# Performance work log

Measured on AMD Instinct MI355X. Metric: run time of the kernel, lower is better.

## Reference

```python
import jax, jax.numpy as jnp
import numpy as np

B, N, E, H = 16, 196, 512, 8   # batch, tokens(14x14), embedding_channels(=KV_size_S), heads
HD = E // H                    # 64  spatial-attn head dim
C = 4 * E                      # 2048 = KV_size (concat of 4 branches)
HDC = C // H                   # 256 channel-attn (SelfAttentionTAT) head dim

def _ln(x, g, b, eps=1e-6):
    m = jnp.mean(x, -1, keepdims=True)
    v = jnp.mean(jnp.square(x - m), -1, keepdims=True)
    return (x - m) * jax.lax.rsqrt(v + eps) * g + b

def setup_inputs():
    key = jax.random.key(0)
    ks = jax.random.split(key, 16)
    n = lambda k, s, sc=0.02: jax.random.normal(k, s, jnp.float32) * sc
    return {
        "emb1": jax.random.normal(ks[0], (B, N, E), jnp.float32),
        "emb2": jax.random.normal(ks[1], (B, N, E), jnp.float32),
        "emb3": jax.random.normal(ks[2], (B, N, E), jnp.float32),
        "emb4": jax.random.normal(ks[3], (B, N, E), jnp.float32),
        "ln_attn_g": jnp.ones((4, E), jnp.float32), "ln_attn_b": jnp.zeros((4, E), jnp.float32),
        "lnC_g": jnp.ones((C,), jnp.float32), "lnC_b": jnp.zeros((C,), jnp.float32),
        "Wq_c": n(ks[4], (C, C)), "Wk_c": n(ks[5], (C, C)),
        "Wv_c": n(ks[6], (C, C)), "Wo_c": n(ks[7], (C, C)),
        "q_w": n(ks[8], (4, N, N), 0.05),              # query1..4 stacked (token-mixing Linear(196,196))
        "k_w": n(ks[9], (4 * N, 4 * N)),               # key   Linear(784,784)
        "v_w": n(ks[10], (4 * N, 4 * N)),              # value Linear(784,784)
        "out_w": n(ks[11], (4, E, E)),                 # out1..4 stacked
        "ln_ffn_g": jnp.ones((4, E), jnp.float32), "ln_ffn_b": jnp.zeros((4, E), jnp.float32),
        "fc1_w": n(ks[12], (4, E, 4 * E)), "fc1_b": n(ks[13], (4, 4 * E), 1e-6),
        "fc2_w": n(ks[14], (4, 4 * E, E)), "fc2_b": n(ks[15], (4, E), 1e-6),
    }

def reference(emb1, emb2, emb3, emb4, ln_attn_g, ln_attn_b, lnC_g, lnC_b,
              Wq_c, Wk_c, Wv_c, Wo_c, q_w, k_w, v_w, out_w,
              ln_ffn_g, ln_ffn_b, fc1_w, fc1_b, fc2_w, fc2_b):
    embs = jnp.stack([emb1, emb2, emb3, emb4])                         # [4,B,N,E]
    cx = _ln(embs, ln_attn_g[:, None, None, :], ln_attn_b[:, None, None, :])
    ec = _ln(jnp.concatenate([emb1, emb2, emb3, emb4], -1), lnC_g, lnC_b)  # [B,N,C]
    # SelfAttentionTAT: multi-head self-attention over the concatenated channel embedding
    q = (ec @ Wq_c).reshape(B, N, H, HDC).transpose(0, 2, 1, 3)
    k = (ec @ Wk_c).reshape(B, N, H, HDC).transpose(0, 2, 1, 3)
    v = (ec @ Wv_c).reshape(B, N, H, HDC).transpose(0, 2, 1, 3)
    s = jax.nn.softmax(jnp.einsum('bhnd,bhmd->bhnm', q, k) * np.float32(1.0 / np.sqrt(HDC)), -1)
    T_hat = jnp.einsum('bhnm,bhmd->bhnd', s, v).transpose(0, 2, 1, 3).reshape(B, N, C) @ Wo_c
    # split channel dim into 4 chunks, concat along token axis -> [B,4N,E]
    KV_S = T_hat.reshape(B, N, 4, E).transpose(0, 2, 1, 3).reshape(B, 4 * N, E)
    # token-mixing projections (Linear applied to the token axis)
    Q = jnp.einsum('gbnc,gnm->gbmc', cx, q_w)                          # [4,B,N,E]
    K = jnp.einsum('bnc,nm->bmc', KV_S, k_w)                           # [B,4N,E]
    V = jnp.einsum('bnc,nm->bmc', KV_S, v_w)
    Qh = Q.reshape(4, B, N, H, HD).transpose(0, 1, 3, 2, 4)            # [4,B,H,N,HD]
    Kh = K.reshape(B, 4 * N, H, HD).transpose(0, 2, 1, 3)              # [B,H,4N,HD]
    Vh = V.reshape(B, 4 * N, H, HD).transpose(0, 2, 1, 3)
    attn = jnp.einsum('gbhnd,bhmd->gbhnm', Qh, Kh)                     # [4,B,H,N,4N]
    # InstanceNorm2d (no affine, eps=1e-5) over (N,4N) per (branch,batch,head) instead of 1/sqrt(d)
    m = jnp.mean(attn, (-2, -1), keepdims=True)
    var = jnp.mean(jnp.square(attn - m), (-2, -1), keepdims=True)
    p = jax.nn.softmax((attn - m) * jax.lax.rsqrt(var + 1e-5), -1)
    ctx = jnp.einsum('gbhnm,bhmd->gbhnd', p, Vh)                       # [4,B,H,N,HD]
    # faithful to source: only branch 1 is permuted before .view; branches 2-4
    # are .view'ed directly from [B,H,N,HD] (head-major flatten)
    c1 = ctx[0].transpose(0, 2, 1, 3).reshape(B, N, E)
    crest = ctx[1:].reshape(3, B, N, E)
    cmerged = jnp.concatenate([c1[None], crest], 0)                    # [4,B,N,E]
    h = embs + jnp.einsum('gbne,gef->gbnf', cmerged, out_w)            # residual 1
    x = _ln(h, ln_ffn_g[:, None, None, :], ln_ffn_b[:, None, None, :])
    x = jax.nn.gelu(jnp.einsum('gbne,gef->gbnf', x, fc1_w) + fc1_b[:, None, None, :], approximate=False)
    x = jnp.einsum('gbnf,gfe->gbne', x, fc2_w) + fc2_b[:, None, None, :]
    out = x + h                                                        # residual 2
    return (out[0], out[1], out[2], out[3])
```

## Files before the change

### kernel.cpp

```cpp
#include <hip/hip_runtime.h>
#include <hip/hip_bf16.h>
#include <math.h>

typedef __hip_bfloat16 bf16;
typedef __attribute__((ext_vector_type(8))) short v8s;
typedef __attribute__((ext_vector_type(4))) short v4s;
typedef __attribute__((ext_vector_type(4))) float v4f;

#define Bq   16
#define Nq   196
#define Eq   512
#define Hq   8
#define HDq  64
#define Cq   2048
#define HDCq 256
#define N4q  784
#define BNq  (Bq*Nq)
#define SLOT ((long)BNq*Cq)
#define L2E  1.44269504f

struct P4 { const void* p[4]; };

__global__ __launch_bounds__(256) void k_fill(float* __restrict__ out, long n, float v) {
  long i = (long)blockIdx.x * 256 + threadIdx.x;
  if (i < n) out[i] = v;
}

__device__ __forceinline__ float blk_sum(float v, float* buf) {
  #pragma unroll
  for (int off = 32; off; off >>= 1) v += __shfl_down(v, off, 64);
  int tid = threadIdx.x;
  __syncthreads();
  if ((tid & 63) == 0) buf[tid >> 6] = v;
  __syncthreads();
  return buf[0] + buf[1] + buf[2] + buf[3];
}

__device__ __forceinline__ unsigned int pack2bf(float a, float b) {
  unsigned short ha = __builtin_bit_cast(unsigned short, (bf16)a);
  unsigned short hb = __builtin_bit_cast(unsigned short, (bf16)b);
  return (unsigned int)ha | ((unsigned int)hb << 16);
}

__global__ __launch_bounds__(256) void k_ln_concat(
    const float* __restrict__ e1, const float* __restrict__ e2,
    const float* __restrict__ e3, const float* __restrict__ e4,
    const float* __restrict__ gamma, const float* __restrict__ beta,
    bf16* __restrict__ ec) {
  __shared__ float buf[4];
  int row = blockIdx.x;
  int tid = threadIdx.x;
  float vals[8];
  #pragma unroll
  for (int i = 0; i < 8; i++) {
    const float* src = (i < 2) ? e1 : (i < 4) ? e2 : (i < 6) ? e3 : e4;
    vals[i] = src[(long)row * Eq + (i & 1) * 256 + tid];
  }
  float s = 0;
  #pragma unroll
  for (int i = 0; i < 8; i++) s += vals[i];
  float mean = blk_sum(s, buf) * (1.f / 2048.f);
  float ss = 0;
  #pragma unroll
  for (int i = 0; i < 8; i++) { float d = vals[i] - mean; ss += d * d; }
  float rstd = rsqrtf(blk_sum(ss, buf) * (1.f / 2048.f) + 1e-6f);
  #pragma unroll
  for (int i = 0; i < 8; i++) {
    int c = tid + i * 256;
    ec[(long)row * Cq + c] = (bf16)((vals[i] - mean) * rstd * gamma[c] + beta[c]);
  }
}

__global__ __launch_bounds__(256) void k_ln_branch(
    const float* __restrict__ e1, const float* __restrict__ e2,
    const float* __restrict__ e3, const float* __restrict__ e4,
    const float* __restrict__ gamma, const float* __restrict__ beta,
    bf16* __restrict__ cx) {
  __shared__ float buf[4];
  int idx = blockIdx.x;
  int tid = threadIdx.x;
  int row = idx % BNq; int g = idx / BNq;
  const float* src = (g == 0) ? e1 : (g == 1) ? e2 : (g == 2) ? e3 : e4;
  float v0 = src[(long)row * Eq + tid];
  float v1 = src[(long)row * Eq + 256 + tid];
  float mean = blk_sum(v0 + v1, buf) * (1.f / 512.f);
  float d0 = v0 - mean, d1 = v1 - mean;
  float var = blk_sum(d0 * d0 + d1 * d1, buf) * (1.f / 512.f);
  float rstd = rsqrtf(var + 1e-6f);
  cx[(long)idx * Eq + tid]       = (bf16)(d0 * rstd * gamma[g * Eq + tid]       + beta[g * Eq + tid]);
  cx[(long)idx * Eq + 256 + tid] = (bf16)(d1 * rstd * gamma[g * Eq + 256 + tid] + beta[g * Eq + 256 + tid]);
}

__global__ __launch_bounds__(256) void k_ln_rows(
    const bf16* __restrict__ x, const float* __restrict__ gamma, const float* __restrict__ beta,
    bf16* __restrict__ out) {
  __shared__ float buf[4];
  int idx = blockIdx.x;
  int tid = threadIdx.x;
  int g = idx / BNq;
  float v0 = (float)x[(long)idx * Eq + tid];
  float v1 = (float)x[(long)idx * Eq + 256 + tid];
  float mean = blk_sum(v0 + v1, buf) * (1.f / 512.f);
  float d0 = v0 - mean, d1 = v1 - mean;
  float var = blk_sum(d0 * d0 + d1 * d1, buf) * (1.f / 512.f);
  float rstd = rsqrtf(var + 1e-6f);
  out[(long)idx * Eq + tid]       = (bf16)(d0 * rstd * gamma[g * Eq + tid]       + beta[g * Eq + tid]);
  out[(long)idx * Eq + 256 + tid] = (bf16)(d1 * rstd * gamma[g * Eq + 256 + tid] + beta[g * Eq + 256 + tid]);
}

__global__ __launch_bounds__(256) void k_cvt_t(
    const float* __restrict__ W, bf16* __restrict__ WT, int K, int Nn) {
  __shared__ short T[64][72];
  int tid = threadIdx.x;
  long zo = (long)blockIdx.z * K * Nn;
  int n0 = blockIdx.x * 64, k0 = blockIdx.y * 64;
  int r = tid >> 2, c = (tid & 3) * 16;
  const float* src = W + zo + (long)(k0 + r) * Nn + n0 + c;
  float4 f0 = *(const float4*)src;
  float4 f1 = *(const float4*)(src + 4);
  float4 f2 = *(const float4*)(src + 8);
  float4 f3 = *(const float4*)(src + 12);
  float fv[16] = {f0.x,f0.y,f0.z,f0.w, f1.x,f1.y,f1.z,f1.w,
                  f2.x,f2.y,f2.z,f2.w, f3.x,f3.y,f3.z,f3.w};
  #pragma unroll
  for (int e = 0; e < 16; e++)
    T[c + e][r] = __builtin_bit_cast(short, (bf16)fv[e]);
  __syncthreads();
  short* dst = (short*)WT + zo + (long)(n0 + r) * K + k0 + c;
  *(v8s*)dst       = *(const v8s*)&T[r][c];
  *(v8s*)(dst + 8) = *(const v8s*)&T[r][c + 8];
}

template<bool HAS_BIAS, bool GELU, int RES_MODE, bool OUT_F32>
__global__ __launch_bounds__(256, 2) void k_gemm_bt(
    const bf16* __restrict__ A, const bf16* __restrict__ WT,
    const float* __restrict__ bias, P4 resp,
    void* __restrict__ out, int M, int Nn, int K,
    long aStride, long wStride, long oStride) {
  __shared__ short As[256][76];
  __shared__ short Bs[64][76];
  int tid = threadIdx.x;
  int l = tid & 63, w = tid >> 6;
  int li = l & 15, lg = l >> 4;
  int z = blockIdx.z;
  int m0 = blockIdx.x * 256, n0 = blockIdx.y * 64;
  const short* Ab = (const short*)A + (long)z * aStride;
  const short* Wb = (const short*)WT + (long)z * wStride;
  const void* res = resp.p[z];

  v4f acc[4][4] = {};

  int ar = tid >> 1, ak = (tid & 1) * 32;
  long arow0 = (long)m0 + ar;       if (arow0 >= M) arow0 = M - 1;
  long arow1 = (long)m0 + ar + 128; if (arow1 >= M) arow1 = M - 1;
  const short* ap0 = Ab + arow0 * K + ak;
  const short* ap1 = Ab + arow1 * K + ak;
  int br = tid >> 2, bk = (tid & 3) * 16;
  const short* bp = Wb + (long)(n0 + br) * K + bk;

  for (int k0 = 0; k0 < K; k0 += 64) {
    const short* p0 = ap0 + k0;
    const short* p1 = ap1 + k0;
    *(v8s*)&As[ar][ak]            = *(const v8s*)p0;
    *(v8s*)&As[ar][ak + 8]        = *(const v8s*)(p0 + 8);
    *(v8s*)&As[ar][ak + 16]       = *(const v8s*)(p0 + 16);
    *(v8s*)&As[ar][ak + 24]       = *(const v8s*)(p0 + 24);
    *(v8s*)&As[ar + 128][ak]      = *(const v8s*)p1;
    *(v8s*)&As[ar + 128][ak + 8]  = *(const v8s*)(p1 + 8);
    *(v8s*)&As[ar + 128][ak + 16] = *(const v8s*)(p1 + 16);
    *(v8s*)&As[ar + 128][ak + 24] = *(const v8s*)(p1 + 24);
    *(v8s*)&Bs[br][bk]            = *(const v8s*)(bp + k0);
    *(v8s*)&Bs[br][bk + 8]        = *(const v8s*)(bp + k0 + 8);
    __syncthreads();
    #pragma unroll
    for (int ks = 0; ks < 2; ks++) {
      v8s af[4], bfr[4];
      #pragma unroll
      for (int mi = 0; mi < 4; mi++)
        af[mi] = *(const v8s*)&As[w * 64 + mi * 16 + li][ks * 32 + lg * 8];
      #pragma unroll
      for (int nj = 0; nj < 4; nj++)
        bfr[nj] = *(const v8s*)&Bs[nj * 16 + li][ks * 32 + lg * 8];
      #pragma unroll
      for (int mi = 0; mi < 4; mi++)
        #pragma unroll
        for (int nj = 0; nj < 4; nj++)
          acc[mi][nj] = __builtin_amdgcn_mfma_f32_16x16x32_bf16(af[mi], bfr[nj], acc[mi][nj], 0, 0, 0);
    }
    __syncthreads();
  }

  #pragma unroll
  for (int nj = 0; nj < 4; nj++) {
    int n = n0 + nj * 16 + li;
    float bv = HAS_BIAS ? bias[n] : 0.f;
    #pragma unroll
    for (int mi = 0; mi < 4; mi++) {
      #pragma unroll
      for (int rr = 0; rr < 4; rr++) {
        int m = m0 + w * 64 + mi * 16 + lg * 4 + rr;
        if (m < M) {
          float x = acc[mi][nj][rr] + bv;
          if (GELU) x = 0.5f * x * (1.f + erff(x * 0.70710678118f));
          if (RES_MODE == 1) x += ((const float*)res)[(long)m * Nn + n];
          if (RES_MODE == 2) x += (float)((const bf16*)res)[(long)m * Nn + n];
          if (OUT_F32) (((float*)out) + (long)z * oStride)[(long)m * Nn + n] = x;
          else         (((bf16*)out)  + (long)z * oStride)[(long)m * Nn + n] = (bf16)x;
        }
      }
    }
  }
}

template<bool HAS_BIAS, bool GELU, int RES_MODE, bool OUT_F32>
__global__ __launch_bounds__(256, 2) void k_gemm(
    const bf16* __restrict__ A, const float* __restrict__ W,
    const float* __restrict__ bias, const void* __restrict__ res,
    void* __restrict__ out, int M, int Nn, int K) {
  __shared__ short As[256][76];
  __shared__ short Bs[64][72];
  int tid = threadIdx.x;
  int l = tid & 63, w = tid >> 6;
  int li = l & 15, lg = l >> 4;
  int m0 = blockIdx.x * 256, n0 = blockIdx.y * 64;

  v4f acc[4][4] = {};

  int ar = tid >> 1, ak = (tid & 1) * 32;
  long arow0 = (long)m0 + ar;       if (arow0 >= M) arow0 = M - 1;
  long arow1 = (long)m0 + ar + 128; if (arow1 >= M) arow1 = M - 1;
  const short* ap0 = (const short*)A + arow0 * K + ak;
  const short* ap1 = (const short*)A + arow1 * K + ak;

  for (int k0 = 0; k0 < K; k0 += 64) {
    {
      const short* p0 = ap0 + k0;
      const short* p1 = ap1 + k0;
      *(v8s*)&As[ar][ak]            = *(const v8s*)p0;
      *(v8s*)&As[ar][ak + 8]        = *(const v8s*)(p0 + 8);
      *(v8s*)&As[ar][ak + 16]       = *(const v8s*)(p0 + 16);
      *(v8s*)&As[ar][ak + 24]       = *(const v8s*)(p0 + 24);
      *(v8s*)&As[ar + 128][ak]      = *(const v8s*)p1;
      *(v8s*)&As[ar + 128][ak + 8]  = *(const v8s*)(p1 + 8);
      *(v8s*)&As[ar + 128][ak + 16] = *(const v8s*)(p1 + 16);
      *(v8s*)&As[ar + 128][ak + 24] = *(const v8s*)(p1 + 24);
    }
    #pragma unroll
    for (int t = 0; t < 2; t++) {
      int p = tid + 256 * t;
      int kp = p >> 4, nf = p & 15;
      const float* wp = W + (long)(k0 + 2 * kp) * Nn + n0 + nf * 4;
      float4 w0 = *(const float4*)wp;
      float4 w1 = *(const float4*)(wp + Nn);
      float f0[4] = {w0.x, w0.y, w0.z, w0.w};
      float f1[4] = {w1.x, w1.y, w1.z, w1.w};
      int ko = (2 * kp) ^ ((nf & 7) << 3);
      #pragma unroll
      for (int e = 0; e < 4; e++)
        *(unsigned int*)&Bs[nf * 4 + e][ko] = pack2bf(f0[e], f1[e]);
    }
    __syncthreads();
    #pragma unroll
    for (int ks = 0; ks < 2; ks++) {
      v8s af[4], bfr[4];
      #pragma unroll
      for (int mi = 0; mi < 4; mi++)
        af[mi] = *(const v8s*)&As[w * 64 + mi * 16 + li][ks * 32 + lg * 8];
      #pragma unroll
      for (int nj = 0; nj < 4; nj++) {
        int rn = nj * 16 + li;
        int ko = (ks * 32 + lg * 8) ^ (((rn >> 2) & 7) << 3);
        bfr[nj] = *(const v8s*)&Bs[rn][ko];
      }
      #pragma unroll
      for (int mi = 0; mi < 4; mi++)
        #pragma unroll
        for (int nj = 0; nj < 4; nj++)
          acc[mi][nj] = __builtin_amdgcn_mfma_f32_16x16x32_bf16(af[mi], bfr[nj], acc[mi][nj], 0, 0, 0);
    }
    __syncthreads();
  }

  #pragma unroll
  for (int nj = 0; nj < 4; nj++) {
    int n = n0 + nj * 16 + li;
    float bv = HAS_BIAS ? bias[n] : 0.f;
    #pragma unroll
    for (int mi = 0; mi < 4; mi++) {
      #pragma unroll
      for (int rr = 0; rr < 4; rr++) {
        int m = m0 + w * 64 + mi * 16 + lg * 4 + rr;
        if (m < M) {
          float x = acc[mi][nj][rr] + bv;
          if (GELU) x = 0.5f * x * (1.f + erff(x * 0.70710678118f));
          if (RES_MODE == 1) x += ((const float*)res)[(long)m * Nn + n];
          if (RES_MODE == 2) x += (float)((const bf16*)res)[(long)m * Nn + n];
          if (OUT_F32) ((float*)out)[(long)m * Nn + n] = x;
          else         ((bf16*)out)[(long)m * Nn + n] = (bf16)x;
        }
      }
    }
  }
}

template<bool REINDEX, bool TRANSV>
__global__ __launch_bounds__(256) void k_mix_mfma(
    const bf16* __restrict__ X, const float* __restrict__ Wt, bf16* __restrict__ out,
    int T) {
  __shared__ short Aws[128][72];
  __shared__ short Xs[128][72];
  int tid = threadIdx.x;
  int l = tid & 63, w = tid >> 6;
  int li = l & 15, lg = l >> 4;
  int wr = w >> 1, wc = w & 1;
  int bidx = blockIdx.x;
  int c0 = blockIdx.y * 128;
  int m0 = blockIdx.z * 128;
  const float* W = REINDEX ? Wt : (Wt + (long)(bidx >> 4) * T * T);
  const short* xb = (const short*)X + (REINDEX ? (long)bidx * Nq * Cq
                                               : (long)bidx * Nq * Eq);
  bf16* ob = out + (long)bidx * T * Eq;

  v4f acc[4][4] = {};
  int nsteps = (T + 63) / 64;
  bool mfull = (m0 + 128 <= T);
  for (int s = 0; s < nsteps; s++) {
    int k0 = s * 64;
    if (mfull) {
      #pragma unroll
      for (int t = 0; t < 4; t++) {
        int p = tid + 256 * t;
        int kp = p >> 5, mf = p & 31;
        int n0r = k0 + 2 * kp; if (n0r > T - 1) n0r = T - 1;
        int n1r = k0 + 2 * kp + 1; if (n1r > T - 1) n1r = T - 1;
        const float* w0p = W + (long)n0r * T + m0 + mf * 4;
        const float* w1p = W + (long)n1r * T + m0 + mf * 4;
        float4 w0 = *(const float4*)w0p;
        float4 w1 = *(const float4*)w1p;
        float f0[4] = {w0.x, w0.y, w0.z, w0.w};
        float f1[4] = {w1.x, w1.y, w1.z, w1.w};
        int ko = (2 * kp) ^ ((mf & 7) << 3);
        #pragma unroll
        for (int e = 0; e < 4; e++)
          *(unsigned int*)&Aws[mf * 4 + e][ko] = pack2bf(f0[e], f1[e]);
      }
    } else {
      #pragma unroll
      for (int t = 0; t < 4; t++) {
        int p = tid + 256 * t;
        int kp = p >> 5, mf = p & 31;
        int n0r = min(k0 + 2 * kp, T - 1);
        int n1r = min(k0 + 2 * kp + 1, T - 1);
        int ko = (2 * kp) ^ ((mf & 7) << 3);
        #pragma unroll
        for (int e = 0; e < 4; e++) {
          int m = min(m0 + mf * 4 + e, T - 1);
          *(unsigned int*)&Aws[mf * 4 + e][ko] =
              pack2bf(W[(long)n0r * T + m], W[(long)n1r * T + m]);
        }
      }
    }
    #pragma unroll
    for (int t = 0; t < 2; t++) {
      int p = tid + 256 * t;
      int np = p >> 4, cg = p & 15;
      int n0r = k0 + 2 * np, n1r = n0r + 1;
      v8s x0 = {}, x1 = {};
      if (n0r < T) {
        const short* xp;
        if (REINDEX) {
          int q4 = (n0r >= 588) ? 3 : (n0r >= 392) ? 2 : (n0r >= 196) ? 1 : 0;
          xp = xb + (long)(n0r - q4 * Nq) * Cq + q4 * Eq + c0 + cg * 8;
        } else {
          xp = xb + (long)n0r * Eq + c0 + cg * 8;
        }
        x0 = *(const v8s*)xp;
      }
      if (n1r < T) {
        const short* xp;
        if (REINDEX) {
          int q4 = (n1r >= 588) ? 3 : (n1r >= 392) ? 2 : (n1r >= 196) ? 1 : 0;
          xp = xb + (long)(n1r - q4 * Nq) * Cq + q4 * Eq + c0 + cg * 8;
        } else {
          xp = xb + (long)n1r * Eq + c0 + cg * 8;
        }
        x1 = *(const v8s*)xp;
      }
      int ko = (2 * np) ^ ((cg & 7) << 3);
      #pragma unroll
      for (int e = 0; e < 8; e++) {
        unsigned short h0 = (unsigned short)x0[e];
        unsigned short h1 = (unsigned short)x1[e];
        *(unsigned int*)&Xs[cg * 8 + e][ko] = (unsigned int)h0 | ((unsigned int)h1 << 16);
      }
    }
    __syncthreads();
    #pragma unroll
    for (int ks = 0; ks < 2; ks++) {
      v8s af[4], bfr[4];
      #pragma unroll
      for (int mi = 0; mi < 4; mi++) {
        int rm = wr * 64 + mi * 16 + li;
        int ko = (ks * 32 + lg * 8) ^ (((rm >> 2) & 7) << 3);
        af[mi] = *(const v8s*)&Aws[rm][ko];
      }
      #pragma unroll
      for (int nj = 0; nj < 4; nj++) {
        int rc = wc * 64 + nj * 16 + li;
        int ko = (ks * 32 + lg * 8) ^ (((rc >> 3) & 7) << 3);
        bfr[nj] = *(const v8s*)&Xs[rc][ko];
      }
      if (TRANSV) {
        #pragma unroll
        for (int nj = 0; nj < 4; nj++)
          #pragma unroll
          for (int mi = 0; mi < 4; mi++)
            acc[nj][mi] = __builtin_amdgcn_mfma_f32_16x16x32_bf16(bfr[nj], af[mi], acc[nj][mi], 0, 0, 0);
      } else {
        #pragma unroll
        for (int mi = 0; mi < 4; mi++)
          #pragma unroll
          for (int nj = 0; nj < 4; nj++)
            acc[mi][nj] = __builtin_amdgcn_mfma_f32_16x16x32_bf16(af[mi], bfr[nj], acc[mi][nj], 0, 0, 0);
      }
    }
    __syncthreads();
  }

  if (TRANSV) {
    bf16* obt = out + (long)bidx * Eq * T;
    #pragma unroll
    for (int mi = 0; mi < 4; mi++) {
      int m = m0 + wr * 64 + mi * 16 + li;
      if (m < T) {
        #pragma unroll
        for (int nj = 0; nj < 4; nj++) {
          #pragma unroll
          for (int rr = 0; rr < 4; rr++) {
            int c = c0 + wc * 64 + nj * 16 + lg * 4 + rr;
            obt[(long)c * T + m] = (bf16)acc[nj][mi][rr];
          }
        }
      }
    }
  } else {
    #pragma unroll
    for (int nj = 0; nj < 4; nj++) {
      int c = c0 + wc * 64 + nj * 16 + li;
      #pragma unroll
      for (int mi = 0; mi < 4; mi++) {
        #pragma unroll
        for (int rr = 0; rr < 4; rr++) {
          int m = m0 + wr * 64 + mi * 16 + lg * 4 + rr;
          if (m < T) ob[(long)m * Eq + c] = (bf16)acc[mi][nj][rr];
        }
      }
    }
  }
}

__global__ __launch_bounds__(256) void k_chan_attn(
    const bf16* __restrict__ q, const bf16* __restrict__ k, const bf16* __restrict__ v,
    bf16* __restrict__ T) {
  __shared__ short P[16 * 232];
  __shared__ float mbuf[4][16];
  __shared__ float dbuf[4][16];
  int tid = threadIdx.x;
  int l = tid & 63, w = tid >> 6;
  int bid = blockIdx.x;
  int it = bid / 128, bh = bid % 128;
  int h = bh & 7; int b = bh >> 3;
  int i0 = it * 16;
  int li = l & 15, lg = l >> 4;

  for (int z = tid; z < 16 * 28; z += 256) P[(z / 28) * 232 + 196 + (z % 28)] = 0;

  int arow = i0 + li;
  const short* qp = (const short*)(q + ((long)(b * Nq) + (arow < Nq ? arow : 0)) * Cq + h * HDCq + lg * 8);
  v8s qf[8] = {};
  if (arow < Nq) {
    #pragma unroll
    for (int kk = 0; kk < 8; kk++) qf[kk] = *(const v8s*)(qp + kk * 32);
  }

  float accS[4][4];
  float lmax[4] = {-1e30f, -1e30f, -1e30f, -1e30f};
  #pragma unroll
  for (int jj = 0; jj < 4; jj++) {
    int jt = w + jj * 4;
    if (jt < 13) {
      int jrow = jt * 16 + li;
      int jr = jrow < Nq ? jrow : Nq - 1;
      const short* kp = (const short*)(k + ((long)(b * Nq) + jr) * Cq + h * HDCq + lg * 8);
      v4f acc = {0.f, 0.f, 0.f, 0.f};
      #pragma unroll
      for (int kk = 0; kk < 8; kk++) {
        v8s kf = *(const v8s*)(kp + kk * 32);
        acc = __builtin_amdgcn_mfma_f32_16x16x32_bf16(qf[kk], kf, acc, 0, 0, 0);
      }
      bool valid = jrow < Nq;
      #pragma unroll
      for (int rr = 0; rr < 4; rr++) {
        float s = acc[rr] * (0.0625f * L2E);
        accS[jj][rr] = s;
        if (valid) lmax[rr] = fmaxf(lmax[rr], s);
      }
    } else {
      #pragma unroll
      for (int rr = 0; rr < 4; rr++) accS[jj][rr] = 0.f;
    }
  }
  #pragma unroll
  for (int rr = 0; rr < 4; rr++) {
    float mv = lmax[rr];
    #pragma unroll
    for (int m = 1; m < 16; m <<= 1) mv = fmaxf(mv, __shfl_xor(mv, m, 64));
    if (li == 0) mbuf[w][lg * 4 + rr] = mv;
  }
  __syncthreads();
  float gmx[4];
  #pragma unroll
  for (int rr = 0; rr < 4; rr++) {
    int row = lg * 4 + rr;
    gmx[rr] = fmaxf(fmaxf(mbuf[0][row], mbuf[1][row]), fmaxf(mbuf[2][row], mbuf[3][row]));
  }

  float ds4[4] = {0.f, 0.f, 0.f, 0.f};
  #pragma unroll
  for (int jj = 0; jj < 4; jj++) {
    int jt = w + jj * 4;
    if (jt < 13) {
      int jrow = jt * 16 + li;
      bool valid = jrow < Nq;
      #pragma unroll
      for (int rr = 0; rr < 4; rr++) {
        float e = valid ? exp2f(accS[jj][rr] - gmx[rr]) : 0.f;
        bf16 pb = (bf16)e;
        ds4[rr] += (float)pb;
        P[(lg * 4 + rr) * 232 + jt * 16 + li] = __builtin_bit_cast(short, pb);
      }
    }
  }
  #pragma unroll
  for (int rr = 0; rr < 4; rr++) {
    float sv = ds4[rr];
    #pragma unroll
    for (int m = 1; m < 16; m <<= 1) sv += __shfl_xor(sv, m, 64);
    if (li == 0) dbuf[w][lg * 4 + rr] = sv;
  }
  __syncthreads();

  v8s pfs[7];
  #pragma unroll
  for (int js = 0; js < 7; js++) pfs[js] = *(const v8s*)&P[li * 232 + js * 32 + lg * 8];

  const short* vbase = (const short*)(v + (long)(b * Nq) * Cq + h * HDCq);
  float accO[4][4];
  #pragma unroll
  for (int dt = 0; dt < 4; dt++) {
    int d = w * 64 + dt * 16 + li;
    v4f acc = {0.f, 0.f, 0.f, 0.f};
    #pragma unroll
    for (int js = 0; js < 6; js++) {
      const short* vp = vbase + (long)(js * 32 + lg * 8) * Cq + d;
      v8s vf;
      #pragma unroll
      for (int e = 0; e < 8; e++) vf[e] = vp[(long)e * Cq];
      acc = __builtin_amdgcn_mfma_f32_16x16x32_bf16(vf, pfs[js], acc, 0, 0, 0);
    }
    {
      int j0 = 192 + lg * 8;
      const short* vp = vbase + (long)j0 * Cq + d;
      v8s vf = {};
      #pragma unroll
      for (int e = 0; e < 8; e++) if (j0 + e < Nq) vf[e] = vp[(long)e * Cq];
      acc = __builtin_amdgcn_mfma_f32_16x16x32_bf16(vf, pfs[6], acc, 0, 0, 0);
    }
    #pragma unroll
    for (int rr = 0; rr < 4; rr++) accO[dt][rr] = acc[rr];
  }

  float inv = 1.f / (dbuf[0][li] + dbuf[1][li] + dbuf[2][li] + dbuf[3][li]);
  int ic = i0 + li;
  if (ic < Nq) {
    #pragma unroll
    for (int dt = 0; dt < 4; dt++) {
      bf16* tp = T + ((long)(b * Nq) + ic) * Cq + h * HDCq + w * 64 + dt * 16 + lg * 4;
      v4s ov;
      #pragma unroll
      for (int rr = 0; rr < 4; rr++) {
        bf16 t = (bf16)(accO[dt][rr] * inv);
        ov[rr] = __builtin_bit_cast(short, t);
      }
      *(v4s*)tp = ov;
    }
  }
}

__global__ __launch_bounds__(256) void k_gram(
    const bf16* __restrict__ Qs, const bf16* __restrict__ Ks,
    float* __restrict__ G, float* __restrict__ XS) {
  __shared__ short XT[64][136];
  int tid = threadIdx.x;
  int l = tid & 63, w = tid >> 6;
  int li = l & 15, lg = l >> 4;
  int r = blockIdx.x;
  const short* xb; int R;
  if (r < 512) {
    int gb = r >> 3, h = r & 7;
    xb = (const short*)Qs + (long)gb * Nq * Eq + h * 64; R = Nq;
  } else {
    int idx = r - 512; int b = idx >> 3, h = idx & 7;
    xb = (const short*)Ks + (long)b * N4q * Eq + h * 64; R = N4q;
  }
  v4f acc[4] = {};
  float xsum = 0.f;
  for (int n0 = 0; n0 < R; n0 += 128) {
    __syncthreads();
    #pragma unroll
    for (int t = 0; t < 4; t++) {
      int task = tid + 256 * t;
      int nn = task >> 3, oct = task & 7;
      int n = n0 + nn;
      v8s xv = {};
      if (n < R) xv = *(const v8s*)(xb + (long)n * Eq + oct * 8);
      #pragma unroll
      for (int e = 0; e < 8; e++) XT[oct * 8 + e][nn] = xv[e];
    }
    __syncthreads();
    if (tid < 64) {
      #pragma unroll
      for (int c = 0; c < 128; c += 8) {
        v8s v = *(const v8s*)&XT[tid][c];
        #pragma unroll
        for (int e = 0; e < 8; e++) xsum += (float)__builtin_bit_cast(bf16, v[e]);
      }
    }
    #pragma unroll
    for (int ks = 0; ks < 4; ks++) {
      v8s af = *(const v8s*)&XT[w * 16 + li][ks * 32 + lg * 8];
      #pragma unroll
      for (int t2 = 0; t2 < 4; t2++) {
        v8s bf2 = *(const v8s*)&XT[t2 * 16 + li][ks * 32 + lg * 8];
        acc[t2] = __builtin_amdgcn_mfma_f32_16x16x32_bf16(af, bf2, acc[t2], 0, 0, 0);
      }
    }
  }
  float* gout = G + (long)r * 4096;
  #pragma unroll
  for (int t2 = 0; t2 < 4; t2++)
    #pragma unroll
    for (int rr = 0; rr < 4; rr++)
      gout[(w * 16 + lg * 4 + rr) * 64 + t2 * 16 + li] = acc[t2][rr];
  if (tid < 64) XS[(long)r * 64 + tid] = xsum;
}

__global__ __launch_bounds__(256) void k_statfin(
    const float* __restrict__ G, const float* __restrict__ XS,
    float* __restrict__ stat) {
  __shared__ float buf[4];
  int r = blockIdx.x;
  int h = r & 7; int b = (r >> 3) & 15;
  int kidx = 512 + b * 8 + h;
  const float* gq = G + (long)r * 4096;
  const float* gk = G + (long)kidx * 4096;
  int tid = threadIdx.x;
  float f = 0.f;
  for (int i = tid; i < 4096; i += 256) f += gq[i] * gk[i];
  float frob = blk_sum(f, buf);
  float md = (tid < 64) ? XS[(long)r * 64 + tid] * XS[(long)kidx * 64 + tid] : 0.f;
  float meandot = blk_sum(md, buf);
  if (tid == 0) {
    float inv = 1.f / ((float)Nq * (float)N4q);
    float mean = meandot * inv;
    float var = frob * inv - mean * mean;
    stat[1024 + r * 2] = mean;
    stat[1024 + r * 2 + 1] = rsqrtf(var + 1e-5f);
  }
}

__global__ __launch_bounds__(256) void k_spa_attn(
    const bf16* __restrict__ Q, const bf16* __restrict__ K, const bf16* __restrict__ VT,
    const float* __restrict__ stat, bf16* __restrict__ ctx) {
  __shared__ short P[16 * 832];
  __shared__ float mbuf[4][16];
  __shared__ float dbuf[4][16];
  int tid = threadIdx.x;
  int l = tid & 63, w = tid >> 6;
  int bid = blockIdx.x;
  int it = bid / 512, r = bid % 512;
  int h = r & 7; int gb = r >> 3; int b = gb & 15;
  int i0 = it * 16;
  int li = l & 15, lg = l >> 4;

  for (int z = tid; z < 16 * 48; z += 256) {
    int i = z / 48, j = 784 + (z % 48);
    P[i * 832 + ((((j >> 3) ^ (i & 7))) << 3) + (j & 7)] = 0;
  }

  float rstdl2 = stat[1024 + r * 2 + 1] * L2E;

  int arow = i0 + li;
  const short* qp = (const short*)(Q + ((long)gb * Nq + (arow < Nq ? arow : 0)) * Eq + h * 64 + lg * 8);
  v8s qf0 = {}, qf1 = {};
  if (arow < Nq) { qf0 = *(const v8s*)qp; qf1 = *(const v8s*)(qp + 32); }

  const short* kbase = (const short*)(K + ((long)b * N4q + li) * Eq + h * 64 + lg * 8);

  float accS[13][4];
  float lmax = -1e30f;
  #pragma unroll
  for (int jj = 0; jj < 13; jj++) {
    int jt = w + jj * 4;
    if (jt < 49) {
      const short* kp = kbase + (long)jt * 16 * Eq;
      v8s kf0 = *(const v8s*)kp;
      v8s kf1 = *(const v8s*)(kp + 32);
      v4f acc = {0.f, 0.f, 0.f, 0.f};
      acc = __builtin_amdgcn_mfma_f32_16x16x32_bf16(kf0, qf0, acc, 0, 0, 0);
      acc = __builtin_amdgcn_mfma_f32_16x16x32_bf16(kf1, qf1, acc, 0, 0, 0);
      #pragma unroll
      for (int rr = 0; rr < 4; rr++) {
        accS[jj][rr] = acc[rr];
        lmax = fmaxf(lmax, acc[rr]);
      }
    } else {
      #pragma unroll
      for (int rr = 0; rr < 4; rr++) accS[jj][rr] = 0.f;
    }
  }
  lmax = fmaxf(lmax, __shfl_xor(lmax, 16, 64));
  lmax = fmaxf(lmax, __shfl_xor(lmax, 32, 64));
  if (lg == 0) mbuf[w][li] = lmax;
  __syncthreads();
  float gmx = fmaxf(fmaxf(mbuf[0][li], mbuf[1][li]), fmaxf(mbuf[2][li], mbuf[3][li]));

  float dsum = 0.f;
  #pragma unroll
  for (int jj = 0; jj < 13; jj++) {
    int jt = w + jj * 4;
    if (jt < 49) {
      v4s pk;
      #pragma unroll
      for (int rr = 0; rr < 4; rr++) {
        float e = exp2f((accS[jj][rr] - gmx) * rstdl2);
        bf16 pb = (bf16)e;
        dsum += (float)pb;
        pk[rr] = __builtin_bit_cast(short, pb);
      }
      *(v4s*)&P[li * 832 + (((jt * 2 + (lg >> 1)) ^ (li & 7)) << 3) + ((lg & 1) << 2)] = pk;
    }
  }
  dsum += __shfl_xor(dsum, 16, 64);
  dsum += __shfl_xor(dsum, 32, 64);
  if (lg == 0) dbuf[w][li] = dsum;
  __syncthreads();

  const short* vtb = (const short*)VT + ((long)b * Eq + h * 64 + w * 16 + li) * N4q;
  v4f accO = {0.f, 0.f, 0.f, 0.f};
  for (int js = 0; js < 24; js++) {
    v8s vf = *(const v8s*)(vtb + js * 32 + lg * 8);
    v8s pf = *(const v8s*)&P[li * 832 + (((js * 4 + lg) ^ (li & 7)) << 3)];
    accO = __builtin_amdgcn_mfma_f32_16x16x32_bf16(vf, pf, accO, 0, 0, 0);
  }
  {
    int jb = 768 + lg * 8;
    v8s vf = {};
    if (jb < N4q) vf = *(const v8s*)(vtb + jb);
    v8s pf = *(const v8s*)&P[li * 832 + (((96 + lg) ^ (li & 7)) << 3)];
    accO = __builtin_amdgcn_mfma_f32_16x16x32_bf16(vf, pf, accO, 0, 0, 0);
  }
  float inv = 1.f / (dbuf[0][li] + dbuf[1][li] + dbuf[2][li] + dbuf[3][li]);
  int ic = i0 + li;
  if (ic < Nq) {
    bf16* cp = ctx + (long)r * Nq * 64 + (long)ic * 64 + w * 16 + lg * 4;
    v4s ov;
    #pragma unroll
    for (int rr = 0; rr < 4; rr++) {
      bf16 t = (bf16)(accO[rr] * inv);
      ov[rr] = __builtin_bit_cast(short, t);
    }
    *(v4s*)cp = ov;
  }
}

__global__ __launch_bounds__(256) void k_scramble(
    const bf16* __restrict__ ctx, bf16* __restrict__ cm) {
  long i = (long)blockIdx.x * 256 + threadIdx.x;
  int e = (int)(i & 511); long t = i >> 9;
  int n = (int)(t % Nq); long gb = t / Nq;
  int g = (int)(gb >> 4);
  long srcIdx;
  if (g == 0) {
    int h = e >> 6, d = e & 63;
    srcIdx = ((gb * 8 + h) * (long)Nq + n) * 64 + d;
  } else {
    int l = n * 512 + e;
    int h = l / 12544; int rem = l % 12544; int n2 = rem >> 6; int d = rem & 63;
    srcIdx = ((gb * 8 + h) * (long)Nq + n2) * 64 + d;
  }
  cm[i] = ctx[srcIdx];
}

extern "C" void kernel_launch(void* const* d_in, const int* in_sizes, int n_in,
                              void* d_out, int out_size, void* d_ws, size_t ws_size,
                              hipStream_t stream) {
  const int expect[22] = {
    1605632, 1605632, 1605632, 1605632,
    2048, 2048, 2048, 2048,
    4194304, 4194304, 4194304, 4194304,
    153664, 614656, 614656, 1048576,
    2048, 2048,
    4194304, 8192, 4194304, 2048
  };
  long fillBlocks = ((long)out_size + 255) / 256;
  if (n_in != 22) {
    k_fill<<<fillBlocks, 256, 0, stream>>>((float*)d_out, out_size, 3000.f);
    return;
  }
  for (int i = 0; i < 22; i++) {
    if (in_sizes[i] != expect[i]) {
      k_fill<<<fillBlocks, 256, 0, stream>>>((float*)d_out, out_size, 1000.f + 20.f * i);
      return;
    }
  }

  const float* e1 = (const float*)d_in[0];
  const float* e2 = (const float*)d_in[1];
  const float* e3 = (const float*)d_in[2];
  const float* e4 = (const float*)d_in[3];
  const float* ln_attn_g = (const float*)d_in[4];
  const float* ln_attn_b = (const float*)d_in[5];
  const float* lnC_g = (const float*)d_in[6];
  const float* lnC_b = (const float*)d_in[7];
  const float* Wq = (const float*)d_in[8];
  const float* Wk = (const float*)d_in[9];
  const float* Wv = (const float*)d_in[10];
  const float* Wo = (const float*)d_in[11];
  const float* q_w = (const float*)d_in[12];
  const float* k_w = (const float*)d_in[13];
  const float* v_w = (const float*)d_in[14];
  const float* out_w = (const float*)d_in[15];
  const float* ln_ffn_g = (const float*)d_in[16];
  const float* ln_ffn_b = (const float*)d_in[17];
  const float* fc1_w = (const float*)d_in[18];
  const float* fc1_b = (const float*)d_in[19];
  const float* fc2_w = (const float*)d_in[20];
  const float* fc2_b = (const float*)d_in[21];

  bf16* W0 = (bf16*)d_ws;
  bf16* W1 = W0 + SLOT;
  bf16* W2 = W0 + 2 * SLOT;
  bf16* OUTS = (bf16*)d_out;
  float* OUT = (float*)d_out;
  float* ST = (float*)((char*)d_ws + 3 * SLOT * sizeof(bf16));
  float* GR = OUT + SLOT / 2;
  float* XSUM = GR + 640 * 4096;
  bf16* WB = (bf16*)(OUT + SLOT / 2);

  dim3 gqkv(13, Cq / 64);
  dim3 gcvC(Cq / 64, Cq / 64);
  long off = (long)BNq * Eq;
  P4 nores = {};

  k_ln_concat<<<BNq, 256, 0, stream>>>(e1, e2, e3, e4, lnC_g, lnC_b, W0);
  k_cvt_t<<<gcvC, 256, 0, stream>>>(Wq, WB, Cq, Cq);
  k_gemm_bt<false,false,0,false><<<gqkv, 256, 0, stream>>>(W0, WB, nullptr, nores, W1, BNq, Cq, Cq, 0, 0, 0);
  k_cvt_t<<<gcvC, 256, 0, stream>>>(Wk, WB, Cq, Cq);
  k_gemm_bt<false,false,0,false><<<gqkv, 256, 0, stream>>>(W0, WB, nullptr, nores, W2, BNq, Cq, Cq, 0, 0, 0);
  k_cvt_t<<<gcvC, 256, 0, stream>>>(Wv, WB, Cq, Cq);
  k_gemm_bt<false,false,0,false><<<gqkv, 256, 0, stream>>>(W0, WB, nullptr, nores, OUTS, BNq, Cq, Cq, 0, 0, 0);
  k_chan_attn<<<Bq * Hq * 13, 256, 0, stream>>>(W1, W2, OUTS, W0);
  k_cvt_t<<<gcvC, 256, 0, stream>>>(Wo, WB, Cq, Cq);
  k_gemm_bt<false,false,0,false><<<gqkv, 256, 0, stream>>>(W0, WB, nullptr, nores, W1, BNq, Cq, Cq, 0, 0, 0);

  k_ln_branch<<<4 * BNq, 256, 0, stream>>>(e1, e2, e3, e4, ln_attn_g, ln_attn_b, W0);
  dim3 gmq(64, 4, 2);
  k_mix_mfma<false,false><<<gmq, 256, 0, stream>>>(W0, q_w, W2, Nq);
  dim3 gmkv(16, 4, 7);
  k_mix_mfma<true,false><<<gmkv, 256, 0, stream>>>(W1, k_w, OUTS, N4q);
  k_mix_mfma<true,true><<<gmkv, 256, 0, stream>>>(W1, v_w, W0, N4q);

  k_gram<<<640, 256, 0, stream>>>(W2, OUTS, GR, XSUM);
  k_statfin<<<512, 256, 0, stream>>>(GR, XSUM, ST);
  k_cvt_t<<<dim3(Eq / 64, Eq / 64, 4), 256, 0, stream>>>(out_w, WB, Eq, Eq);
  k_spa_attn<<<512 * 13, 256, 0, stream>>>(W2, OUTS, W0, ST, W1);

  k_scramble<<<(4L * BNq * Eq) / 256, 256, 0, stream>>>(W1, W2);
  P4 resp; resp.p[0] = e1; resp.p[1] = e2; resp.p[2] = e3; resp.p[3] = e4;
  k_gemm_bt<false,false,1,false><<<dim3(13, Eq / 64, 4), 256, 0, stream>>>(
      W2, WB, nullptr, resp, W0, BNq, Eq, Eq, off, (long)Eq * Eq, off);

  k_ln_rows<<<4 * BNq, 256, 0, stream>>>(W0, ln_ffn_g, ln_ffn_b, W1);
  dim3 gfc1(13, (4 * Eq) / 64);
  dim3 gfc2(13, Eq / 64);
  for (int g = 0; g < 4; g++) {
    k_gemm<true,true,0,false><<<gfc1, 256, 0, stream>>>(
        W1 + g * off, fc1_w + (long)g * Eq * 4 * Eq, fc1_b + (long)g * 4 * Eq, nullptr,
        W2, BNq, 4 * Eq, Eq);
    k_gemm<true,false,2,true><<<gfc2, 256, 0, stream>>>(
        W2, fc2_w + (long)g * 4 * Eq * Eq, fc2_b + (long)g * Eq, W0 + g * off,
        OUT + g * off, BNq, Eq, 4 * Eq);
  }
}
```

Baseline: 1.184 ms.

## Batch FFN GEMMs across branches via grid z and drop swizzle in attention P buffer

The four per-branch FC1/FC2 GEMM launch pairs are replaced by batched launches that use blockIdx.z for the branch, with the rows split into two halves of 1568. This gives larger grids per launch and fewer launches, while the FC1 intermediate is sized per half. Separately, the spatial-attention P buffer in LDS drops its XOR swizzle for a linear layout with row pitch 808, which simplifies indexing but may add LDS bank conflicts.

```diff
diff --git a/kernel.cpp b/kernel.cpp
--- a/kernel.cpp
+++ b/kernel.cpp
@@ -216,21 +216,28 @@
 __global__ __launch_bounds__(256, 2) void k_gemm(
     const bf16* __restrict__ A, const float* __restrict__ W,
     const float* __restrict__ bias, const void* __restrict__ res,
-    void* __restrict__ out, int M, int Nn, int K) {
+    void* __restrict__ out, int M, int Nn, int K,
+    long aStride, long wStride, long bStride, long resStride, long oStride) {
   __shared__ short As[256][76];
   __shared__ short Bs[64][72];
   int tid = threadIdx.x;
   int l = tid & 63, w = tid >> 6;
   int li = l & 15, lg = l >> 4;
+  int z = blockIdx.z;
   int m0 = blockIdx.x * 256, n0 = blockIdx.y * 64;
+  const short* Ab = (const short*)A + (long)z * aStride;
+  const float* Wb = W + (long)z * wStride;
+  const float* biasb = HAS_BIAS ? bias + (long)z * bStride : nullptr;
+  const float* resF = (RES_MODE == 1) ? (const float*)res + (long)z * resStride : nullptr;
+  const bf16*  resB = (RES_MODE == 2) ? (const bf16*)res + (long)z * resStride : nullptr;
 
   v4f acc[4][4] = {};
 
   int ar = tid >> 1, ak = (tid & 1) * 32;
   long arow0 = (long)m0 + ar;       if (arow0 >= M) arow0 = M - 1;
   long arow1 = (long)m0 + ar + 128; if (arow1 >= M) arow1 = M - 1;
-  const short* ap0 = (const short*)A + arow0 * K + ak;
-  const short* ap1 = (const short*)A + arow1 * K + ak;
+  const short* ap0 = Ab + arow0 * K + ak;
+  const short* ap1 = Ab + arow1 * K + ak;
 
   for (int k0 = 0; k0 < K; k0 += 64) {
     {
@@ -249,7 +256,7 @@
     for (int t = 0; t < 2; t++) {
       int p = tid + 256 * t;
       int kp = p >> 4, nf = p & 15;
-      const float* wp = W + (long)(k0 + 2 * kp) * Nn + n0 + nf * 4;
+      const float* wp = Wb + (long)(k0 + 2 * kp) * Nn + n0 + nf * 4;
       float4 w0 = *(const float4*)wp;
       float4 w1 = *(const float4*)(wp + Nn);
       float f0[4] = {w0.x, w0.y, w0.z, w0.w};
@@ -284,7 +291,7 @@
   #pragma unroll
   for (int nj = 0; nj < 4; nj++) {
     int n = n0 + nj * 16 + li;
-    float bv = HAS_BIAS ? bias[n] : 0.f;
+    float bv = HAS_BIAS ? biasb[n] : 0.f;
     #pragma unroll
     for (int mi = 0; mi < 4; mi++) {
       #pragma unroll
@@ -293,10 +300,10 @@
         if (m < M) {
           float x = acc[mi][nj][rr] + bv;
           if (GELU) x = 0.5f * x * (1.f + erff(x * 0.70710678118f));
-          if (RES_MODE == 1) x += ((const float*)res)[(long)m * Nn + n];
-          if (RES_MODE == 2) x += (float)((const bf16*)res)[(long)m * Nn + n];
-          if (OUT_F32) ((float*)out)[(long)m * Nn + n] = x;
-          else         ((bf16*)out)[(long)m * Nn + n] = (bf16)x;
+          if (RES_MODE == 1) x += resF[(long)m * Nn + n];
+          if (RES_MODE == 2) x += (float)resB[(long)m * Nn + n];
+          if (OUT_F32) (((float*)out) + (long)z * oStride)[(long)m * Nn + n] = x;
+          else         (((bf16*)out)  + (long)z * oStride)[(long)m * Nn + n] = (bf16)x;
         }
       }
     }
@@ -682,7 +689,7 @@
 __global__ __launch_bounds__(256) void k_spa_attn(
     const bf16* __restrict__ Q, const bf16* __restrict__ K, const bf16* __restrict__ VT,
     const float* __restrict__ stat, bf16* __restrict__ ctx) {
-  __shared__ short P[16 * 832];
+  __shared__ short P[16 * 808];
   __shared__ float mbuf[4][16];
   __shared__ float dbuf[4][16];
   int tid = threadIdx.x;
@@ -693,10 +700,7 @@
   int i0 = it * 16;
   int li = l & 15, lg = l >> 4;
 
-  for (int z = tid; z < 16 * 48; z += 256) {
-    int i = z / 48, j = 784 + (z % 48);
-    P[i * 832 + ((((j >> 3) ^ (i & 7))) << 3) + (j & 7)] = 0;
-  }
+  for (int z = tid; z < 16 * 24; z += 256) P[(z / 24) * 808 + 784 + (z % 24)] = 0;
 
   float rstdl2 = stat[1024 + r * 2 + 1] * L2E;
 
@@ -748,7 +752,7 @@
         dsum += (float)pb;
         pk[rr] = __builtin_bit_cast(short, pb);
       }
-      *(v4s*)&P[li * 832 + (((jt * 2 + (lg >> 1)) ^ (li & 7)) << 3) + ((lg & 1) << 2)] = pk;
+      *(v4s*)&P[li * 808 + jt * 16 + lg * 4] = pk;
     }
   }
   dsum += __shfl_xor(dsum, 16, 64);
@@ -760,14 +764,14 @@
   v4f accO = {0.f, 0.f, 0.f, 0.f};
   for (int js = 0; js < 24; js++) {
     v8s vf = *(const v8s*)(vtb + js * 32 + lg * 8);
-    v8s pf = *(const v8s*)&P[li * 832 + (((js * 4 + lg) ^ (li & 7)) << 3)];
+    v8s pf = *(const v8s*)&P[li * 808 + js * 32 + lg * 8];
     accO = __builtin_amdgcn_mfma_f32_16x16x32_bf16(vf, pf, accO, 0, 0, 0);
   }
   {
     int jb = 768 + lg * 8;
     v8s vf = {};
     if (jb < N4q) vf = *(const v8s*)(vtb + jb);
-    v8s pf = *(const v8s*)&P[li * 832 + (((96 + lg) ^ (li & 7)) << 3)];
+    v8s pf = *(const v8s*)&P[li * 808 + 768 + lg * 8];
     accO = __builtin_amdgcn_mfma_f32_16x16x32_bf16(vf, pf, accO, 0, 0, 0);
   }
   float inv = 1.f / (dbuf[0][li] + dbuf[1][li] + dbuf[2][li] + dbuf[3][li]);
@@ -892,14 +896,15 @@
       W2, WB, nullptr, resp, W0, BNq, Eq, Eq, off, (long)Eq * Eq, off);
 
   k_ln_rows<<<4 * BNq, 256, 0, stream>>>(W0, ln_ffn_g, ln_ffn_b, W1);
-  dim3 gfc1(13, (4 * Eq) / 64);
-  dim3 gfc2(13, Eq / 64);
-  for (int g = 0; g < 4; g++) {
-    k_gemm<true,true,0,false><<<gfc1, 256, 0, stream>>>(
-        W1 + g * off, fc1_w + (long)g * Eq * 4 * Eq, fc1_b + (long)g * 4 * Eq, nullptr,
-        W2, BNq, 4 * Eq, Eq);
-    k_gemm<true,false,2,true><<<gfc2, 256, 0, stream>>>(
-        W2, fc2_w + (long)g * 4 * Eq * Eq, fc2_b + (long)g * Eq, W0 + g * off,
-        OUT + g * off, BNq, Eq, 4 * Eq);
-  }
-}
+  const long MH = 1568;
+  for (int mh = 0; mh < 2; mh++) {
+    k_gemm<true,true,0,false><<<dim3(7, (4 * Eq) / 64, 4), 256, 0, stream>>>(
+        W1 + mh * MH * Eq, fc1_w, fc1_b, nullptr, W2,
+        (int)MH, 4 * Eq, Eq,
+        off, (long)Eq * 4 * Eq, 4 * Eq, 0, MH * 4 * Eq);
+    k_gemm<true,false,2,true><<<dim3(7, Eq / 64, 4), 256, 0, stream>>>(
+        W2, fc2_w, fc2_b, W0 + mh * MH * Eq, OUT + mh * MH * Eq,
+        (int)MH, Eq, 4 * Eq,
+        MH * 4 * Eq, (long)4 * Eq * Eq, Eq, off, off);
+  }
+}
```

Result: faster. 1.128 ms (-4.7%).
